# Kernel tuning notes

Measured on AMD Instinct MI355X. Metric: run time of the kernel, lower is better.

The kernel has to match this reference:

```python
import jax, jax.numpy as jnp
import numpy as np

NUM_EXPERTS = 8
IN_FEATURES = 1024
OUT_FEATURES = 1024
TOP_K = 2


def setup_inputs() -> dict:
    key = jax.random.key(0)
    k_x, k_we, k_be, k_wg, k_bg = jax.random.split(key, 5)
    scale_e = 1.0 / np.sqrt(IN_FEATURES)
    x = jax.random.normal(k_x, (4, 2048, IN_FEATURES), dtype=jnp.float32)
    # expert weights stored torch-style [E, out, in], bias [E, out]
    W_experts = jax.random.uniform(k_we, (NUM_EXPERTS, OUT_FEATURES, IN_FEATURES), minval=-scale_e, maxval=scale_e, dtype=jnp.float32)
    b_experts = jax.random.uniform(k_be, (NUM_EXPERTS, OUT_FEATURES), minval=-scale_e, maxval=scale_e, dtype=jnp.float32)
    W_gate = jax.random.uniform(k_wg, (NUM_EXPERTS, IN_FEATURES), minval=-scale_e, maxval=scale_e, dtype=jnp.float32)
    b_gate = jax.random.uniform(k_bg, (NUM_EXPERTS,), minval=-scale_e, maxval=scale_e, dtype=jnp.float32)
    return {"x": x, "W_experts": W_experts, "b_experts": b_experts, "W_gate": W_gate, "b_gate": b_gate}


def reference(x, W_experts, b_experts, W_gate, b_gate):
    B, S, D = x.shape
    x_flat = x.reshape(-1, D)  # [T, D]
    # gating
    gate_logits = x_flat @ W_gate.T + b_gate  # [T, E]
    topk_vals, topk_idxs = jax.lax.top_k(gate_logits, TOP_K)  # [T, K]
    topk_weights = jax.nn.softmax(topk_vals, axis=-1)  # [T, K]
    # dense per-token per-expert weight via one-hot scatter of top-k weights
    one_hot = jax.nn.one_hot(topk_idxs, NUM_EXPERTS, dtype=x.dtype)  # [T, K, E]
    w = jnp.einsum('tke,tk->te', one_hot, topk_weights)  # [T, E]
    # every expert runs densely over all tokens (faithful to source)
    expert_outs = jnp.einsum('td,efd->tef', x_flat, W_experts) + b_experts  # [T, E, F]
    out_flat = jnp.einsum('te,tef->tf', w, expert_outs)  # [T, F]
    return out_flat.reshape(B, S, -1)
```

## Files before the change

### kernel.cpp

```cpp
#include <hip/hip_runtime.h>
#include <hip/hip_bf16.h>
#include <stdint.h>

#define NE 8
#define DK 1024
#define FN 1024
#define NTOK 8192

#define BM 320
#define BN 256
#define BK 64
#define NIT (DK / BK)
#define MT 52

#define HB 32
#define EPB (NTOK * 2 / HB)

#define BUFS 73728
#define BOFF 40960

typedef __attribute__((ext_vector_type(4))) float f32x4;
typedef __attribute__((ext_vector_type(8))) short short8;
typedef __attribute__((ext_vector_type(4))) short short4v;

__device__ __forceinline__ unsigned short f2bf(float f) {
    union { float f; unsigned u; } v; v.f = f;
    unsigned r = v.u;
    unsigned lsb = (r >> 16) & 1u;
    r += 0x7fffu + lsb;
    return (unsigned short)(r >> 16);
}
__device__ __forceinline__ float bf2f(unsigned short u) {
    union { unsigned u; float f; } v; v.u = ((unsigned)u) << 16;
    return v.f;
}

__global__ __launch_bounds__(256) void k_gate(const float* __restrict__ x,
    const float* __restrict__ Wg, const float* __restrict__ bg,
    unsigned short* __restrict__ xb, int* __restrict__ meta_e,
    float* __restrict__ meta_w)
{
    const int lane = threadIdx.x & 63;
    const int t = blockIdx.x * 4 + (threadIdx.x >> 6);

    const f32x4* xr = (const f32x4*)(x + (size_t)t * DK);
    f32x4 xv[4];
#pragma unroll
    for (int c = 0; c < 4; ++c) xv[c] = xr[lane + 64 * c];

    short4v* xbo = (short4v*)(xb + (size_t)t * DK);
#pragma unroll
    for (int c = 0; c < 4; ++c) {
        short4v b;
        b.x = (short)f2bf(xv[c].x); b.y = (short)f2bf(xv[c].y);
        b.z = (short)f2bf(xv[c].z); b.w = (short)f2bf(xv[c].w);
        xbo[lane + 64 * c] = b;
    }

    float acc[NE];
#pragma unroll
    for (int e = 0; e < NE; ++e) {
        const f32x4* wr = (const f32x4*)(Wg + e * DK);
        float a = 0.f;
#pragma unroll
        for (int c = 0; c < 4; ++c) {
            f32x4 wv = wr[lane + 64 * c];
            a += xv[c].x * wv.x + xv[c].y * wv.y + xv[c].z * wv.z + xv[c].w * wv.w;
        }
        acc[e] = a;
    }
#pragma unroll
    for (int e = 0; e < NE; ++e) {
        float a = acc[e];
#pragma unroll
        for (int off = 32; off > 0; off >>= 1) a += __shfl_xor(a, off, 64);
        acc[e] = a;
    }
    if (lane == 0) {
        float v[NE];
#pragma unroll
        for (int e = 0; e < NE; ++e) v[e] = acc[e] + bg[e];
        int b0 = 0; float m0 = v[0];
#pragma unroll
        for (int e = 1; e < NE; ++e) if (v[e] > m0) { m0 = v[e]; b0 = e; }
        int b1 = -1; float m1 = -3.4e38f;
#pragma unroll
        for (int e = 0; e < NE; ++e) if (e != b0 && v[e] > m1) { m1 = v[e]; b1 = e; }
        float r = expf(m1 - m0);
        float s = 1.f + r;
        meta_e[2 * t] = b0; meta_e[2 * t + 1] = b1;
        meta_w[2 * t] = 1.f / s; meta_w[2 * t + 1] = r / s;
    }
}

__global__ __launch_bounds__(256) void k_convw(const float* __restrict__ W,
                                               unsigned short* __restrict__ Wb)
{
    int i = blockIdx.x * 256 + threadIdx.x;
    f32x4 v = ((const f32x4*)W)[i];
    short4v b;
    b.x = (short)f2bf(v.x); b.y = (short)f2bf(v.y);
    b.z = (short)f2bf(v.z); b.w = (short)f2bf(v.w);
    ((short4v*)Wb)[i] = b;
}

__global__ __launch_bounds__(256) void k_hist(const int* __restrict__ meta_e,
                                              int* __restrict__ blockcnt)
{
    __shared__ int lh[NE];
    if (threadIdx.x < NE) lh[threadIdx.x] = 0;
    __syncthreads();
    int base = blockIdx.x * EPB;
#pragma unroll
    for (int k = 0; k < EPB / 256; ++k)
        atomicAdd(&lh[meta_e[base + k * 256 + threadIdx.x]], 1);
    __syncthreads();
    if (threadIdx.x < NE) blockcnt[blockIdx.x * NE + threadIdx.x] = lh[threadIdx.x];
}

__global__ void k_scan(const int* __restrict__ blockcnt, int* __restrict__ seg,
                       int* __restrict__ base)
{
    __shared__ int pre[HB][NE];
    __shared__ int colsum[NE];
    __shared__ int segstart[NE];
    int tid = threadIdx.x;
    if (tid < NE) {
        int run = 0;
        for (int b = 0; b < HB; ++b) { pre[b][tid] = run; run += blockcnt[b * NE + tid]; }
        colsum[tid] = run;
    }
    __syncthreads();
    if (tid == 0) {
        int s = 0;
        for (int e = 0; e < NE; ++e) { segstart[e] = s; seg[e] = s; s += colsum[e]; }
        seg[NE] = s;
    }
    __syncthreads();
    for (int i = tid; i < HB * NE; i += 64) {
        int b = i / NE, e = i % NE;
        base[i] = segstart[e] + pre[b][e];
    }
}

__global__ __launch_bounds__(256) void k_scatter(const int* __restrict__ meta_e,
    const float* __restrict__ meta_w, const int* __restrict__ base,
    int* __restrict__ ridx, float* __restrict__ rw)
{
    __shared__ int lh[NE];
    __shared__ int bb[NE];
    if (threadIdx.x < NE) {
        lh[threadIdx.x] = 0;
        bb[threadIdx.x] = base[blockIdx.x * NE + threadIdx.x];
    }
    __syncthreads();
    int bs = blockIdx.x * EPB;
#pragma unroll
    for (int k = 0; k < EPB / 256; ++k) {
        int i = bs + k * 256 + threadIdx.x;
        int e = meta_e[i];
        int r = atomicAdd(&lh[e], 1);
        int p = bb[e] + r;
        ridx[p] = i;
        rw[p] = meta_w[i];
    }
}

template <int MODE>
__global__ __launch_bounds__(512, 2) void k_gemm(const unsigned short* __restrict__ xb,
    const unsigned short* __restrict__ Wb, const float* __restrict__ be,
    const int* __restrict__ seg, const int* __restrict__ ridx,
    const float* __restrict__ rw, float* __restrict__ out, void* __restrict__ ywv)
{
    __shared__ char Lds[2 * BUFS];

    const int bid = blockIdx.x;
    const int e = bid & 7;
    const int n0 = ((bid >> 3) & 3) * BN;
    const int mt = bid >> 5;
    const int s0 = seg[e];
    const int L = seg[e + 1] - s0;
    const int m0 = mt * BM;
    if (m0 >= L) return;

    const int tid = threadIdx.x;
    const int lane = tid & 63;
    const int wid = tid >> 6;
    const int wm = wid >> 2, wn = wid & 3;

    const int ag = ((tid & 7) ^ ((tid >> 3) & 7)) * 8;
    const unsigned short* asrc[5];
#pragma unroll
    for (int c = 0; c < 5; ++c) {
        int r = c * 64 + (tid >> 3);
        int idx = m0 + r; if (idx >= L) idx = L - 1;
        asrc[c] = xb + (size_t)(ridx[s0 + idx] >> 1) * DK + ag;
    }
    const int bgr = ((tid & 3) ^ ((tid >> 3) & 3)) * 8;
    const unsigned short* bsrc[2];
#pragma unroll
    for (int c = 0; c < 2; ++c) {
        int r = c * 128 + (tid >> 2);
        bsrc[c] = Wb + ((size_t)e * FN + n0 + r) * DK + bgr;
    }

    char* LB = (char*)Lds;

    f32x4 acc[10][4];
#pragma unroll
    for (int i = 0; i < 10; ++i)
#pragma unroll
        for (int j = 0; j < 4; ++j) acc[i][j] = f32x4{0.f, 0.f, 0.f, 0.f};

    const int frow = lane & 15;
    const int fq = lane >> 4;
    int a_off[10][2], b_off[4][2];
#pragma unroll
    for (int mi = 0; mi < 10; ++mi) {
        int r = wm * 160 + mi * 16 + frow;
#pragma unroll
        for (int kk = 0; kk < 2; ++kk)
            a_off[mi][kk] = r * 128 + (((kk * 4 + fq) ^ (r & 7)) * 16);
    }
#pragma unroll
    for (int ni = 0; ni < 4; ++ni) {
        int r = wn * 64 + ni * 16 + frow;
        int sl = fq ^ ((r >> 1) & 3);
#pragma unroll
        for (int kk = 0; kk < 2; ++kk)
            b_off[ni][kk] = BOFF + kk * 16384 + r * 64 + sl * 16;
    }

    auto STAGE_A = [&](int buf, int kt) {
        const int ko = kt * BK;
        char* dst = LB + buf * BUFS + wid * 1024;
#pragma unroll
        for (int c = 0; c < 5; ++c)
            __builtin_amdgcn_global_load_lds(
                (const __attribute__((address_space(1))) void*)(asrc[c] + ko),
                (__attribute__((address_space(3))) void*)(dst + c * 8192), 16, 0, 0);
    };
    auto STAGE_B = [&](int buf, int kt, int kh) {
        const int ko = kt * BK + kh * 32;
        char* dst = LB + buf * BUFS + BOFF + kh * 16384 + wid * 1024;
#pragma unroll
        for (int c = 0; c < 2; ++c)
            __builtin_amdgcn_global_load_lds(
                (const __attribute__((address_space(1))) void*)(bsrc[c] + ko),
                (__attribute__((address_space(3))) void*)(dst + c * 8192), 16, 0, 0);
    };

#define GATE(N) do { asm volatile("s_waitcnt vmcnt(" #N ")" ::: "memory"); \
                     __builtin_amdgcn_s_barrier(); \
                     __builtin_amdgcn_sched_barrier(0); } while (0)

    STAGE_A(0, 0); STAGE_B(0, 0, 0); STAGE_B(0, 0, 1);
    __builtin_amdgcn_sched_barrier(0);

    for (int t = 0; t < NIT; ++t) {
        const int b = t & 1;
        const char* Cb = LB + b * BUFS;
        const bool st = (t + 1 < NIT);

        GATE(2);
        short8 b0f[4], a0f[10];
#pragma unroll
        for (int ni = 0; ni < 4; ++ni) b0f[ni] = *(const short8*)(Cb + b_off[ni][0]);
#pragma unroll
        for (int mi = 0; mi < 10; ++mi) a0f[mi] = *(const short8*)(Cb + a_off[mi][0]);
        if (st) { STAGE_A(b ^ 1, t + 1); STAGE_B(b ^ 1, t + 1, 0); }
        __builtin_amdgcn_s_setprio(1);
#pragma unroll
        for (int mi = 0; mi < 10; ++mi)
#pragma unroll
            for (int ni = 0; ni < 4; ++ni)
                acc[mi][ni] = __builtin_amdgcn_mfma_f32_16x16x32_bf16(
                    a0f[mi], b0f[ni], acc[mi][ni], 0, 0, 0);
        __builtin_amdgcn_s_setprio(0);

        if (st) { GATE(7); } else { GATE(0); }
        short8 b1f[4], a1f[10];
#pragma unroll
        for (int ni = 0; ni < 4; ++ni) b1f[ni] = *(const short8*)(Cb + b_off[ni][1]);
#pragma unroll
        for (int mi = 0; mi < 10; ++mi) a1f[mi] = *(const short8*)(Cb + a_off[mi][1]);
        if (st) STAGE_B(b ^ 1, t + 1, 1);
        __builtin_amdgcn_s_setprio(1);
#pragma unroll
        for (int mi = 0; mi < 10; ++mi)
#pragma unroll
            for (int ni = 0; ni < 4; ++ni)
                acc[mi][ni] = __builtin_amdgcn_mfma_f32_16x16x32_bf16(
                    a1f[mi], b1f[ni], acc[mi][ni], 0, 0, 0);
        __builtin_amdgcn_s_setprio(0);
    }
#undef GATE

    float bias_n[4];
#pragma unroll
    for (int ni = 0; ni < 4; ++ni)
        bias_n[ni] = be[e * FN + n0 + wn * 64 + ni * 16 + frow];

    const int fq4 = fq * 4;
#pragma unroll
    for (int mi = 0; mi < 10; ++mi) {
        int rl = m0 + wm * 160 + mi * 16 + fq4;
#pragma unroll
        for (int j = 0; j < 4; ++j) {
            int idx = rl + j;
            if (idx < L) {
                float w = rw[s0 + idx];
                int oi = ridx[s0 + idx];
                if (MODE == 0) {
                    float* orow = out + (size_t)(oi >> 1) * FN + n0 + wn * 64 + frow;
#pragma unroll
                    for (int ni = 0; ni < 4; ++ni)
                        atomicAdd(orow + ni * 16, w * (acc[mi][ni][j] + bias_n[ni]));
                } else if (MODE == 1) {
                    short4v pk;
                    pk.x = (short)f2bf(w * (acc[mi][0][j] + bias_n[0]));
                    pk.y = (short)f2bf(w * (acc[mi][1][j] + bias_n[1]));
                    pk.z = (short)f2bf(w * (acc[mi][2][j] + bias_n[2]));
                    pk.w = (short)f2bf(w * (acc[mi][3][j] + bias_n[3]));
                    *(short4v*)((unsigned short*)ywv + (size_t)oi * FN + n0 + wn * 64 + frow * 4) = pk;
                } else {
                    f32x4 pk;
                    pk.x = w * (acc[mi][0][j] + bias_n[0]);
                    pk.y = w * (acc[mi][1][j] + bias_n[1]);
                    pk.z = w * (acc[mi][2][j] + bias_n[2]);
                    pk.w = w * (acc[mi][3][j] + bias_n[3]);
                    *(f32x4*)((float*)ywv + (size_t)oi * FN + n0 + wn * 64 + frow * 4) = pk;
                }
            }
        }
    }
}

__global__ __launch_bounds__(256) void k_combine_bf(const unsigned short* __restrict__ yw,
                                                    float* __restrict__ out)
{
    __shared__ float ls[FN];
    int t = blockIdx.x, i = threadIdx.x;
    const unsigned* r0 = (const unsigned*)(yw + (size_t)(2 * t) * FN);
    const unsigned* r1 = (const unsigned*)(yw + (size_t)(2 * t + 1) * FN);
    unsigned a0 = r0[2 * i], a1 = r0[2 * i + 1];
    unsigned c0 = r1[2 * i], c1 = r1[2 * i + 1];
    float s0 = bf2f((unsigned short)(a0 & 0xffff)) + bf2f((unsigned short)(c0 & 0xffff));
    float s1 = bf2f((unsigned short)(a0 >> 16))    + bf2f((unsigned short)(c0 >> 16));
    float s2 = bf2f((unsigned short)(a1 & 0xffff)) + bf2f((unsigned short)(c1 & 0xffff));
    float s3 = bf2f((unsigned short)(a1 >> 16))    + bf2f((unsigned short)(c1 >> 16));
    int base = (i >> 4) * 64 + (i & 15);
    ls[base +  0] = s0;
    ls[base + 16] = s1;
    ls[base + 32] = s2;
    ls[base + 48] = s3;
    __syncthreads();
    ((f32x4*)(out + (size_t)t * FN))[i] = ((const f32x4*)ls)[i];
}

__global__ __launch_bounds__(256) void k_combine_f32(const float* __restrict__ yw,
                                                     float* __restrict__ out)
{
    __shared__ float ls[FN];
    int t = blockIdx.x, i = threadIdx.x;
    f32x4 a = ((const f32x4*)(yw + (size_t)(2 * t) * FN))[i];
    f32x4 b = ((const f32x4*)(yw + (size_t)(2 * t + 1) * FN))[i];
    f32x4 s = a + b;
    int base = (i >> 4) * 64 + (i & 15);
    ls[base +  0] = s.x;
    ls[base + 16] = s.y;
    ls[base + 32] = s.z;
    ls[base + 48] = s.w;
    __syncthreads();
    ((f32x4*)(out + (size_t)t * FN))[i] = ((const f32x4*)ls)[i];
}

extern "C" void kernel_launch(void* const* d_in, const int* in_sizes, int n_in,
                              void* d_out, int out_size, void* d_ws, size_t ws_size,
                              hipStream_t stream)
{
    const float* x   = (const float*)d_in[0];
    const float* We  = (const float*)d_in[1];
    const float* beb = (const float*)d_in[2];
    const float* Wg  = (const float*)d_in[3];
    const float* bg  = (const float*)d_in[4];
    float* out = (float*)d_out;

    char* ws = (char*)d_ws;
    unsigned short* xb = (unsigned short*)ws;
    unsigned short* Wb = (unsigned short*)(ws + (size_t)(16 << 20));
    size_t off = (size_t)(32 << 20);
    int*   seg      = (int*)(ws + off);   off += 256;
    int*   blockcnt = (int*)(ws + off);   off += HB * NE * 4;
    int*   basebuf  = (int*)(ws + off);   off += HB * NE * 4;
    int*   meta_e   = (int*)(ws + off);   off += (size_t)NTOK * 2 * 4;
    float* meta_w   = (float*)(ws + off); off += (size_t)NTOK * 2 * 4;
    int*   ridxb    = (int*)(ws + off);   off += (size_t)NTOK * 2 * 4;
    float* rwb      = (float*)(ws + off); off += (size_t)NTOK * 2 * 4;
    void*  yw       = (void*)(ws + ((off + 255) & ~(size_t)255));
    size_t yw_base  = (size_t)((off + 255) & ~(size_t)255);

    int mode;
    if (ws_size >= yw_base + (size_t)NTOK * 2 * FN * 2) mode = 1;
    else if (ws_size >= yw_base + (size_t)NTOK * 2 * FN * 4) mode = 2;
    else mode = 0;

    k_gate<<<NTOK / 4, 256, 0, stream>>>(x, Wg, bg, xb, meta_e, meta_w);
    k_convw<<<(NE * FN * DK / 4) / 256, 256, 0, stream>>>(We, Wb);
    k_hist<<<HB, 256, 0, stream>>>(meta_e, blockcnt);
    k_scan<<<1, 64, 0, stream>>>(blockcnt, seg, basebuf);
    k_scatter<<<HB, 256, 0, stream>>>(meta_e, meta_w, basebuf, ridxb, rwb);

    const int nblk = NE * (FN / BN) * MT;
    if (mode == 1) {
        k_gemm<1><<<nblk, 512, 0, stream>>>(xb, Wb, beb, seg, ridxb, rwb, out, yw);
        k_combine_bf<<<NTOK, 256, 0, stream>>>((const unsigned short*)yw, out);
    } else if (mode == 2) {
        k_gemm<2><<<nblk, 512, 0, stream>>>(xb, Wb, beb, seg, ridxb, rwb, out, yw);
        k_combine_f32<<<NTOK, 256, 0, stream>>>((const float*)yw, out);
    } else {
        hipMemsetAsync(d_out, 0, (size_t)NTOK * FN * 4, stream);
        k_gemm<0><<<nblk, 512, 0, stream>>>(xb, Wb, beb, seg, ridxb, rwb, out, yw);
    }
}
```

Baseline: 87.94 us.

## Split each K-half MFMA phase into two M-halves with extra barriers

The inner GEMM loop now loads A fragments five rows at a time instead of ten, with an explicit LDS wait and an extra workgroup barrier between the two M-halves. The global-to-LDS staging of A and of the first B half is spread across these sub-phases instead of being issued together. The aim is lower register pressure and a finer interleave of staging with MFMA work, which may improve occupancy or scheduling. The cost is extra barriers and lgkmcnt(0) stalls that serialize the LDS reads with compute.

```diff
diff --git a/kernel.cpp b/kernel.cpp
--- a/kernel.cpp
+++ b/kernel.cpp
@@ -253,6 +253,20 @@
 #define GATE(N) do { asm volatile("s_waitcnt vmcnt(" #N ")" ::: "memory"); \
                      __builtin_amdgcn_s_barrier(); \
                      __builtin_amdgcn_sched_barrier(0); } while (0)
+#define BARP  do { __builtin_amdgcn_s_barrier(); \
+                   __builtin_amdgcn_sched_barrier(0); } while (0)
+#define LGKM0 do { asm volatile("s_waitcnt lgkmcnt(0)" ::: "memory"); \
+                   __builtin_amdgcn_sched_barrier(0); } while (0)
+#define MFMA5(AF, BF, MLO) do { \
+    __builtin_amdgcn_s_setprio(1); \
+    _Pragma("unroll") \
+    for (int mi = 0; mi < 5; ++mi) { \
+        _Pragma("unroll") \
+        for (int ni = 0; ni < 4; ++ni) \
+            acc[(MLO) + mi][ni] = __builtin_amdgcn_mfma_f32_16x16x32_bf16( \
+                AF[mi], BF[ni], acc[(MLO) + mi][ni], 0, 0, 0); \
+    } \
+    __builtin_amdgcn_s_setprio(0); } while (0)
 
     STAGE_A(0, 0); STAGE_B(0, 0, 0); STAGE_B(0, 0, 1);
     __builtin_amdgcn_sched_barrier(0);
@@ -261,40 +275,43 @@
         const int b = t & 1;
         const char* Cb = LB + b * BUFS;
         const bool st = (t + 1 < NIT);
+        short8 b0f[4], b1f[4], af[5];
 
         GATE(2);
-        short8 b0f[4], a0f[10];
 #pragma unroll
         for (int ni = 0; ni < 4; ++ni) b0f[ni] = *(const short8*)(Cb + b_off[ni][0]);
 #pragma unroll
-        for (int mi = 0; mi < 10; ++mi) a0f[mi] = *(const short8*)(Cb + a_off[mi][0]);
-        if (st) { STAGE_A(b ^ 1, t + 1); STAGE_B(b ^ 1, t + 1, 0); }
-        __builtin_amdgcn_s_setprio(1);
-#pragma unroll
-        for (int mi = 0; mi < 10; ++mi)
-#pragma unroll
-            for (int ni = 0; ni < 4; ++ni)
-                acc[mi][ni] = __builtin_amdgcn_mfma_f32_16x16x32_bf16(
-                    a0f[mi], b0f[ni], acc[mi][ni], 0, 0, 0);
-        __builtin_amdgcn_s_setprio(0);
+        for (int mi = 0; mi < 5; ++mi) af[mi] = *(const short8*)(Cb + a_off[mi][0]);
+        if (st) STAGE_A(b ^ 1, t + 1);
+        LGKM0;
+        MFMA5(af, b0f, 0);
+
+        BARP;
+#pragma unroll
+        for (int mi = 0; mi < 5; ++mi) af[mi] = *(const short8*)(Cb + a_off[5 + mi][0]);
+        if (st) STAGE_B(b ^ 1, t + 1, 0);
+        LGKM0;
+        MFMA5(af, b0f, 5);
 
         if (st) { GATE(7); } else { GATE(0); }
-        short8 b1f[4], a1f[10];
 #pragma unroll
         for (int ni = 0; ni < 4; ++ni) b1f[ni] = *(const short8*)(Cb + b_off[ni][1]);
 #pragma unroll
-        for (int mi = 0; mi < 10; ++mi) a1f[mi] = *(const short8*)(Cb + a_off[mi][1]);
+        for (int mi = 0; mi < 5; ++mi) af[mi] = *(const short8*)(Cb + a_off[mi][1]);
         if (st) STAGE_B(b ^ 1, t + 1, 1);
-        __builtin_amdgcn_s_setprio(1);
-#pragma unroll
-        for (int mi = 0; mi < 10; ++mi)
-#pragma unroll
-            for (int ni = 0; ni < 4; ++ni)
-                acc[mi][ni] = __builtin_amdgcn_mfma_f32_16x16x32_bf16(
-                    a1f[mi], b1f[ni], acc[mi][ni], 0, 0, 0);
-        __builtin_amdgcn_s_setprio(0);
+        LGKM0;
+        MFMA5(af, b1f, 0);
+
+        BARP;
+#pragma unroll
+        for (int mi = 0; mi < 5; ++mi) af[mi] = *(const short8*)(Cb + a_off[5 + mi][1]);
+        LGKM0;
+        MFMA5(af, b1f, 5);
     }
 #undef GATE
+#undef BARP
+#undef LGKM0
+#undef MFMA5
 
     float bias_n[4];
 #pragma unroll
```

After: 88.24 us. Within noise of the previous version (+0.3%).
